# Optimization experiments

Hardware: AMD Instinct MI355X
Metric: run time of the kernel (lower is better)

## Reference

```python
import jax, jax.numpy as jnp
import numpy as np

B, T, D, DH, DFF = 4, 2048, 1024, 1024, 4096


def setup_inputs() -> dict:
    key = jax.random.key(0)
    ks = jax.random.split(key, 8)
    s = 0.02
    return {
        "x": jax.random.normal(ks[0], (B, T, D), jnp.float32),
        "ln1_g": jnp.ones((D,), jnp.float32),
        "ln1_b": jnp.zeros((D,), jnp.float32),
        "W_q": jax.random.normal(ks[1], (D, DH), jnp.float32) * s,
        "b_q": jnp.zeros((DH,), jnp.float32),
        "W_k": jax.random.normal(ks[2], (D, DH), jnp.float32) * s,
        "b_k": jnp.zeros((DH,), jnp.float32),
        "W_v": jax.random.normal(ks[3], (D, DH), jnp.float32) * s,
        "b_v": jnp.zeros((DH,), jnp.float32),
        "ln2_g": jnp.ones((D,), jnp.float32),
        "ln2_b": jnp.zeros((D,), jnp.float32),
        "W_in": jax.random.normal(ks[4], (D, DFF), jnp.float32) * s,
        "b_in": jnp.zeros((DFF,), jnp.float32),
        "W_out": jax.random.normal(ks[5], (DFF, D), jnp.float32) * s,
        "b_out": jnp.zeros((D,), jnp.float32),
    }


def _layernorm(x, g, b, eps=1e-5):
    mu = jnp.mean(x, axis=-1, keepdims=True)
    var = jnp.var(x, axis=-1, keepdims=True)
    return (x - mu) * jax.lax.rsqrt(var + eps) * g + b


def reference(x, ln1_g, ln1_b, W_q, b_q, W_k, b_k, W_v, b_v,
              ln2_g, ln2_b, W_in, b_in, W_out, b_out):
    # --- attention branch (pre-LN) ---
    h = _layernorm(x, ln1_g, ln1_b)                      # [B,T,D]
    Q = h @ W_q + b_q                                    # [B,T,DH]
    K = h @ W_k + b_k
    V = h @ W_v + b_v
    scale = 1.0 / jnp.sqrt(jnp.asarray(K.shape[-1], h.dtype))
    att = jnp.einsum("btd,bsd->bts", Q, K) * scale       # [B,T,T]
    # NOTE: source calls att.masked_fill(...) without assignment -> mask
    # is discarded; faithfully no causal mask applied here.
    att = jax.nn.softmax(att, axis=-1)
    attn_out = jnp.einsum("bts,bsd->btd", att, V)        # [B,T,DH]
    x = x + attn_out
    # --- MLP branch (pre-LN) ---
    h2 = _layernorm(x, ln2_g, ln2_b)
    ff = jax.nn.gelu(h2 @ W_in + b_in, approximate=False)
    x = x + (ff @ W_out + b_out)
    return x
```

## Files before the change

### kernel.cpp

```cpp
#include <hip/hip_runtime.h>
#include <hip/hip_bf16.h>

#define B_    4
#define T_    2048
#define D_    1024
#define DH_   1024
#define DFF_  4096
#define MTOT  (B_ * T_)

using f32x4  = __attribute__((ext_vector_type(4))) float;
using bf16x8 = __attribute__((ext_vector_type(8))) short;

__device__ __forceinline__ unsigned short f2bf(float f) {
    unsigned u = __builtin_bit_cast(unsigned, f);
    u += 0x7fffu + ((u >> 16) & 1u);
    return (unsigned short)(u >> 16);
}

__device__ __forceinline__ void gload16(const short* g, short* l) {
    __builtin_amdgcn_global_load_lds(
        (const __attribute__((address_space(1))) unsigned int*)g,
        (__attribute__((address_space(3))) unsigned int*)l, 16, 0, 0);
}

__global__ __launch_bounds__(256) void transp_f32_bf16(
    const float* __restrict__ src, short* __restrict__ dst, int K, int N) {
    __shared__ float tile[32][33];
    int tk = blockIdx.y * 32, tn = blockIdx.x * 32;
    int tx = threadIdx.x & 31, ty = threadIdx.x >> 5;
#pragma unroll
    for (int i = 0; i < 4; i++) {
        int r = ty + i * 8;
        tile[r][tx] = src[(size_t)(tk + r) * N + tn + tx];
    }
    __syncthreads();
#pragma unroll
    for (int i = 0; i < 4; i++) {
        int r = ty + i * 8;
        dst[(size_t)(tn + r) * K + tk + tx] = f2bf(tile[tx][r]);
    }
}

__global__ void copyv(const float* __restrict__ s, float* __restrict__ d, int n) {
    int i = blockIdx.x * blockDim.x + threadIdx.x;
    if (i < n) d[i] = s[i];
}

__global__ __launch_bounds__(256) void ln_rows(
    const float* __restrict__ x, const float* __restrict__ g,
    const float* __restrict__ bta, short* __restrict__ out) {
    int row = blockIdx.x;
    const float* xr = x + (size_t)row * D_;
    int t = threadIdx.x;
    float4 v = *(const float4*)(xr + t * 4);
    float s  = v.x + v.y + v.z + v.w;
    float s2 = v.x * v.x + v.y * v.y + v.z * v.z + v.w * v.w;
#pragma unroll
    for (int off = 1; off < 64; off <<= 1) {
        s  += __shfl_xor(s, off);
        s2 += __shfl_xor(s2, off);
    }
    __shared__ float as_[4], as2_[4];
    int wave = t >> 6, lane = t & 63;
    if (lane == 0) { as_[wave] = s; as2_[wave] = s2; }
    __syncthreads();
    s  = as_[0] + as_[1] + as_[2] + as_[3];
    s2 = as2_[0] + as2_[1] + as2_[2] + as2_[3];
    float mean = s * (1.0f / D_);
    float var  = s2 * (1.0f / D_) - mean * mean;
    float rstd = rsqrtf(var + 1e-5f);
    float4 gv = *(const float4*)(g + t * 4);
    float4 bv = *(const float4*)(bta + t * 4);
    short4 o;
    o.x = f2bf((v.x - mean) * rstd * gv.x + bv.x);
    o.y = f2bf((v.y - mean) * rstd * gv.y + bv.y);
    o.z = f2bf((v.z - mean) * rstd * gv.z + bv.z);
    o.w = f2bf((v.w - mean) * rstd * gv.w + bv.w);
    *(short4*)(out + (size_t)row * D_ + t * 4) = o;
}

__global__ __launch_bounds__(256) void softmax_rows(float* __restrict__ S) {
    size_t row = blockIdx.x;
    float* sr = S + row * (size_t)T_;
    int t = threadIdx.x;
    float4 v0 = *(const float4*)(sr + t * 4);
    float4 v1 = *(const float4*)(sr + 1024 + t * 4);
    const float c = 0.03125f;
    float vv[8] = {v0.x * c, v0.y * c, v0.z * c, v0.w * c,
                   v1.x * c, v1.y * c, v1.z * c, v1.w * c};
    float mx = -1e30f;
#pragma unroll
    for (int i = 0; i < 8; i++) mx = fmaxf(mx, vv[i]);
#pragma unroll
    for (int off = 1; off < 64; off <<= 1) mx = fmaxf(mx, __shfl_xor(mx, off));
    __shared__ float sm_[4], ss[4];
    int wave = t >> 6, lane = t & 63;
    if (lane == 0) sm_[wave] = mx;
    __syncthreads();
    mx = fmaxf(fmaxf(sm_[0], sm_[1]), fmaxf(sm_[2], sm_[3]));
    float sum = 0.f;
#pragma unroll
    for (int i = 0; i < 8; i++) { vv[i] = expf(vv[i] - mx); sum += vv[i]; }
#pragma unroll
    for (int off = 1; off < 64; off <<= 1) sum += __shfl_xor(sum, off);
    if (lane == 0) ss[wave] = sum;
    __syncthreads();
    sum = ss[0] + ss[1] + ss[2] + ss[3];
    float inv = 1.0f / sum;
    short* pr = (short*)sr;
    short4 oa, ob;
    oa.x = f2bf(vv[0] * inv); oa.y = f2bf(vv[1] * inv);
    oa.z = f2bf(vv[2] * inv); oa.w = f2bf(vv[3] * inv);
    ob.x = f2bf(vv[4] * inv); ob.y = f2bf(vv[5] * inv);
    ob.z = f2bf(vv[6] * inv); ob.w = f2bf(vv[7] * inv);
    *(short4*)(pr + t * 4) = oa;
    *(short4*)(pr + 1024 + t * 4) = ob;
}

#define TILE_SH 16384
template<int BIAS_MODE, int ACT, int RES, int OUT_BF16>
__global__ __launch_bounds__(512, 2) void gemm8(
    const short* __restrict__ A, int lda, long long sA,
    const short* __restrict__ Bt, int ldb, long long sB,
    void* __restrict__ C, int ldc, long long sC,
    const float* __restrict__ bias,
    const float* __restrict__ res, int ldr, long long sR,
    int K) {
    extern __shared__ short smem_[];
    short* shA = smem_;
    short* shB = smem_ + 2 * TILE_SH;

    int gx = gridDim.x, gy = gridDim.y;
    int n2d = gx * gy;
    int nwg = n2d * gridDim.z;
    int lid = blockIdx.x + gx * (blockIdx.y + gy * blockIdx.z);
    int q = nwg >> 3, rq = nwg & 7, xcd = lid & 7, i_ = lid >> 3;
    int nid = (xcd < rq ? xcd * (q + 1) : rq * (q + 1) + (xcd - rq) * q) + i_;
    int z = nid / n2d, r2d = nid % n2d;
    int sw = gy << 2;
    int strip = r2d / sw, rr = r2d % sw;
    int by = rr >> 2, bx = (strip << 2) + (rr & 3);

    int bm = by * 256, bn = bx * 256;
    const short* gA = A  + (size_t)z * sA + (size_t)bm * lda;
    const short* gB = Bt + (size_t)z * sB + (size_t)bn * ldb;
    int tid = threadIdx.x, lane = tid & 63, w = tid >> 6;
    int wr = w >> 2, wc = w & 3;

    int rbase = tid >> 3;
    int colb  = ((tid << 4) & 127) ^ ((rbase & 7) << 4);
    int col   = colb >> 1;
    const short* pA[4]; const short* pB[4];
#pragma unroll
    for (int c = 0; c < 4; c++) {
        pA[c] = gA + (size_t)(c * 64 + rbase) * lda + col;
        pB[c] = gB + (size_t)(c * 64 + rbase) * ldb + col;
    }
    int aoff[8], boff[4];
#pragma unroll
    for (int f = 0; f < 8; f++) {
        int row = wr * 128 + f * 16 + (lane & 15);
        aoff[f] = row * 128 + ((((lane >> 4) * 16)) ^ ((row & 7) << 4));
    }
#pragma unroll
    for (int f = 0; f < 4; f++) {
        int row = wc * 64 + f * 16 + (lane & 15);
        boff[f] = row * 128 + ((((lane >> 4) * 16)) ^ ((row & 7) << 4));
    }

    int nk = K >> 6;
    f32x4 acc[8][4] = {};

#pragma unroll
    for (int c = 0; c < 4; c++) {
        gload16(pA[c], shA + c * 4096 + tid * 8);
        gload16(pB[c], shB + c * 4096 + tid * 8);
    }
    asm volatile("s_waitcnt vmcnt(0)" ::: "memory");
    __builtin_amdgcn_s_barrier();

#define MF(r_, av) \
    acc[r_][0] = __builtin_amdgcn_mfma_f32_16x16x32_bf16(av, b0, acc[r_][0], 0, 0, 0); \
    acc[r_][1] = __builtin_amdgcn_mfma_f32_16x16x32_bf16(av, b1, acc[r_][1], 0, 0, 0); \
    acc[r_][2] = __builtin_amdgcn_mfma_f32_16x16x32_bf16(av, b2, acc[r_][2], 0, 0, 0); \
    acc[r_][3] = __builtin_amdgcn_mfma_f32_16x16x32_bf16(av, b3, acc[r_][3], 0, 0, 0);

    for (int t = 0; t < nk; t++) {
        const char* sA_ = (const char*)(shA + (t & 1) * TILE_SH);
        const char* sB_ = (const char*)(shB + (t & 1) * TILE_SH);
        short* wA = shA + ((t + 1) & 1) * TILE_SH;
        short* wB = shB + ((t + 1) & 1) * TILE_SH;
        int ks = (t + 1 < nk ? t + 1 : nk - 1) << 6;

        bf16x8 a0 = *(const bf16x8*)(sA_ + aoff[0]);
        bf16x8 a1 = *(const bf16x8*)(sA_ + aoff[1]);
        bf16x8 a2 = *(const bf16x8*)(sA_ + aoff[2]);
        bf16x8 a3 = *(const bf16x8*)(sA_ + aoff[3]);
        bf16x8 b0 = *(const bf16x8*)(sB_ + boff[0]);
        bf16x8 b1 = *(const bf16x8*)(sB_ + boff[1]);
        bf16x8 b2 = *(const bf16x8*)(sB_ + boff[2]);
        bf16x8 b3 = *(const bf16x8*)(sB_ + boff[3]);
        gload16(pA[0] + ks, wA + tid * 8);
        gload16(pA[2] + ks, wA + 2 * 4096 + tid * 8);
        __builtin_amdgcn_s_barrier();
        asm volatile("s_waitcnt lgkmcnt(0)" ::: "memory");
        __builtin_amdgcn_s_setprio(1);
        MF(0, a0) MF(1, a1) MF(2, a2) MF(3, a3)
        __builtin_amdgcn_s_setprio(0);
        asm volatile("s_waitcnt vmcnt(2)" ::: "memory");
        __builtin_amdgcn_s_barrier();

        a0 = *(const bf16x8*)(sA_ + aoff[4]);
        a1 = *(const bf16x8*)(sA_ + aoff[5]);
        a2 = *(const bf16x8*)(sA_ + aoff[6]);
        a3 = *(const bf16x8*)(sA_ + aoff[7]);
        gload16(pB[0] + ks, wB + tid * 8);
        gload16(pB[1] + ks, wB + 4096 + tid * 8);
        __builtin_amdgcn_s_barrier();
        asm volatile("s_waitcnt lgkmcnt(0)" ::: "memory");
        __builtin_amdgcn_s_setprio(1);
        MF(4, a0) MF(5, a1) MF(6, a2) MF(7, a3)
        __builtin_amdgcn_s_setprio(0);
        __builtin_amdgcn_s_barrier();

        a0 = *(const bf16x8*)(sA_ + (aoff[0] ^ 64));
        a1 = *(const bf16x8*)(sA_ + (aoff[1] ^ 64));
        a2 = *(const bf16x8*)(sA_ + (aoff[2] ^ 64));
        a3 = *(const bf16x8*)(sA_ + (aoff[3] ^ 64));
        b0 = *(const bf16x8*)(sB_ + (boff[0] ^ 64));
        b1 = *(const bf16x8*)(sB_ + (boff[1] ^ 64));
        b2 = *(const bf16x8*)(sB_ + (boff[2] ^ 64));
        b3 = *(const bf16x8*)(sB_ + (boff[3] ^ 64));
        gload16(pB[2] + ks, wB + 2 * 4096 + tid * 8);
        gload16(pB[3] + ks, wB + 3 * 4096 + tid * 8);
        __builtin_amdgcn_s_barrier();
        asm volatile("s_waitcnt lgkmcnt(0)" ::: "memory");
        __builtin_amdgcn_s_setprio(1);
        MF(0, a0) MF(1, a1) MF(2, a2) MF(3, a3)
        __builtin_amdgcn_s_setprio(0);
        __builtin_amdgcn_s_barrier();

        a0 = *(const bf16x8*)(sA_ + (aoff[4] ^ 64));
        a1 = *(const bf16x8*)(sA_ + (aoff[5] ^ 64));
        a2 = *(const bf16x8*)(sA_ + (aoff[6] ^ 64));
        a3 = *(const bf16x8*)(sA_ + (aoff[7] ^ 64));
        gload16(pA[1] + ks, wA + 4096 + tid * 8);
        gload16(pA[3] + ks, wA + 3 * 4096 + tid * 8);
        __builtin_amdgcn_s_barrier();
        asm volatile("s_waitcnt lgkmcnt(0)" ::: "memory");
        __builtin_amdgcn_s_setprio(1);
        MF(4, a0) MF(5, a1) MF(6, a2) MF(7, a3)
        __builtin_amdgcn_s_setprio(0);
        asm volatile("s_waitcnt vmcnt(2)" ::: "memory");
        __builtin_amdgcn_s_barrier();
    }
#undef MF
    asm volatile("s_waitcnt vmcnt(0)" ::: "memory");

    size_t zc = (size_t)z * (size_t)sC;
#pragma unroll
    for (int fr = 0; fr < 8; fr++) {
#pragma unroll
        for (int fn = 0; fn < 4; fn++) {
            int colc = bn + wc * 64 + fn * 16 + (lane & 15);
#pragma unroll
            for (int r_ = 0; r_ < 4; r_++) {
                int row = bm + wr * 128 + fr * 16 + (lane >> 4) * 4 + r_;
                float v = acc[fr][fn][r_];
                if (BIAS_MODE == 1) v += bias[colc];
                else if (BIAS_MODE == 2) v += bias[row];
                if (ACT == 1) v = 0.5f * v * (1.0f + erff(v * 0.70710678118654752f));
                if (RES) v += res[(size_t)z * sR + (size_t)row * ldr + colc];
                if (OUT_BF16) ((short*)C)[zc + (size_t)row * ldc + colc] = f2bf(v);
                else          ((float*)C)[zc + (size_t)row * ldc + colc] = v;
            }
        }
    }
}

#define SHBYTES (4 * TILE_SH * 2)

extern "C" void kernel_launch(void* const* d_in, const int* in_sizes, int n_in,
                              void* d_out, int out_size, void* d_ws, size_t ws_size,
                              hipStream_t stream) {
    const float* x    = (const float*)d_in[0];
    const float* ln1g = (const float*)d_in[1];
    const float* ln1b = (const float*)d_in[2];
    const float* Wq   = (const float*)d_in[3];
    const float* bq   = (const float*)d_in[4];
    const float* Wk   = (const float*)d_in[5];
    const float* bk   = (const float*)d_in[6];
    const float* Wv   = (const float*)d_in[7];
    const float* bv   = (const float*)d_in[8];
    const float* ln2g = (const float*)d_in[9];
    const float* ln2b = (const float*)d_in[10];
    const float* Win  = (const float*)d_in[11];
    const float* bin  = (const float*)d_in[12];
    const float* Wout = (const float*)d_in[13];
    const float* bout = (const float*)d_in[14];

    char* ws = (char*)d_ws;
    size_t off = 0;
    auto alloc = [&](size_t bytes) {
        void* p = ws + off;
        off += (bytes + 255) & ~(size_t)255;
        return p;
    };
    short* WqkT  = (short*)alloc((size_t)2048 * 1024 * 2);
    short* WvT   = (short*)alloc((size_t)1024 * 1024 * 2);
    short* WinT  = (short*)alloc((size_t)4096 * 1024 * 2);
    short* WoutT = (short*)alloc((size_t)1024 * 4096 * 2);
    float* bqk   = (float*)alloc((size_t)2048 * 4);
    short* h     = (short*)alloc((size_t)MTOT * 1024 * 2);
    short* QK    = (short*)alloc((size_t)MTOT * 2048 * 2);
    short* VT    = (short*)alloc((size_t)1024 * 8192 * 2);
    float* S     = (float*)alloc((size_t)4 * 2048 * 2048 * 4);
    float* x1    = (float*)alloc((size_t)MTOT * 1024 * 4);
    (void)ws_size; (void)in_sizes; (void)n_in; (void)out_size;

    hipFuncSetAttribute((const void*)gemm8<1,0,0,1>, hipFuncAttributeMaxDynamicSharedMemorySize, SHBYTES);
    hipFuncSetAttribute((const void*)gemm8<2,0,0,1>, hipFuncAttributeMaxDynamicSharedMemorySize, SHBYTES);
    hipFuncSetAttribute((const void*)gemm8<0,0,0,0>, hipFuncAttributeMaxDynamicSharedMemorySize, SHBYTES);
    hipFuncSetAttribute((const void*)gemm8<0,0,1,0>, hipFuncAttributeMaxDynamicSharedMemorySize, SHBYTES);
    hipFuncSetAttribute((const void*)gemm8<1,1,0,1>, hipFuncAttributeMaxDynamicSharedMemorySize, SHBYTES);
    hipFuncSetAttribute((const void*)gemm8<1,0,1,0>, hipFuncAttributeMaxDynamicSharedMemorySize, SHBYTES);

    transp_f32_bf16<<<dim3(32, 32), 256, 0, stream>>>(Wq, WqkT, 1024, 1024);
    transp_f32_bf16<<<dim3(32, 32), 256, 0, stream>>>(Wk, WqkT + (size_t)1024 * 1024, 1024, 1024);
    transp_f32_bf16<<<dim3(32, 32), 256, 0, stream>>>(Wv, WvT, 1024, 1024);
    transp_f32_bf16<<<dim3(128, 32), 256, 0, stream>>>(Win, WinT, 1024, 4096);
    transp_f32_bf16<<<dim3(32, 128), 256, 0, stream>>>(Wout, WoutT, 4096, 1024);
    copyv<<<4, 256, 0, stream>>>(bq, bqk, 1024);
    copyv<<<4, 256, 0, stream>>>(bk, bqk + 1024, 1024);

    ln_rows<<<MTOT, 256, 0, stream>>>(x, ln1g, ln1b, h);

    gemm8<1, 0, 0, 1><<<dim3(8, 32, 1), 512, SHBYTES, stream>>>(
        h, 1024, 0, WqkT, 1024, 0, QK, 2048, 0, bqk, nullptr, 0, 0, 1024);

    gemm8<2, 0, 0, 1><<<dim3(32, 4, 1), 512, SHBYTES, stream>>>(
        WvT, 1024, 0, h, 1024, 0, VT, 8192, 0, bv, nullptr, 0, 0, 1024);

    gemm8<0, 0, 0, 0><<<dim3(8, 8, 4), 512, SHBYTES, stream>>>(
        QK, 2048, 4194304LL, QK + 1024, 2048, 4194304LL,
        S, 2048, 4194304LL, nullptr, nullptr, 0, 0, 1024);

    softmax_rows<<<MTOT, 256, 0, stream>>>(S);

    gemm8<0, 0, 1, 0><<<dim3(4, 8, 4), 512, SHBYTES, stream>>>(
        (short*)S, 4096, 8388608LL, VT, 8192, 2048LL,
        x1, 1024, 2097152LL, nullptr, x, 1024, 2097152LL, 2048);

    ln_rows<<<MTOT, 256, 0, stream>>>(x1, ln2g, ln2b, h);

    short* ff = (short*)S;
    gemm8<1, 1, 0, 1><<<dim3(16, 32, 1), 512, SHBYTES, stream>>>(
        h, 1024, 0, WinT, 1024, 0, ff, 4096, 0, bin, nullptr, 0, 0, 1024);

    gemm8<1, 0, 1, 0><<<dim3(4, 32, 1), 512, SHBYTES, stream>>>(
        ff, 4096, 0, WoutT, 4096, 0, (float*)d_out, 1024, 0, bout,
        x1, 1024, 0, 4096);
}
```

Baseline: 432.7 us.

## Add narrow-N triple-buffered GEMM variant and write attention scores as bf16

```diff
diff --git a/kernel.cpp b/kernel.cpp
--- a/kernel.cpp
+++ b/kernel.cpp
@@ -15,6 +15,10 @@
     unsigned u = __builtin_bit_cast(unsigned, f);
     u += 0x7fffu + ((u >> 16) & 1u);
     return (unsigned short)(u >> 16);
+}
+__device__ __forceinline__ float bf2f(unsigned short h) {
+    unsigned u = ((unsigned)h) << 16;
+    return __builtin_bit_cast(float, u);
 }
 
 __device__ __forceinline__ void gload16(const short* g, short* l) {
@@ -79,15 +83,17 @@
     *(short4*)(out + (size_t)row * D_ + t * 4) = o;
 }
 
-__global__ __launch_bounds__(256) void softmax_rows(float* __restrict__ S) {
+__global__ __launch_bounds__(256) void softmax_rows_bf16(short* __restrict__ S) {
     size_t row = blockIdx.x;
-    float* sr = S + row * (size_t)T_;
+    short* sr = S + row * 4096;
     int t = threadIdx.x;
-    float4 v0 = *(const float4*)(sr + t * 4);
-    float4 v1 = *(const float4*)(sr + 1024 + t * 4);
+    short4 u0 = *(const short4*)(sr + t * 4);
+    short4 u1 = *(const short4*)(sr + 1024 + t * 4);
     const float c = 0.03125f;
-    float vv[8] = {v0.x * c, v0.y * c, v0.z * c, v0.w * c,
-                   v1.x * c, v1.y * c, v1.z * c, v1.w * c};
+    float vv[8] = {bf2f((unsigned short)u0.x) * c, bf2f((unsigned short)u0.y) * c,
+                   bf2f((unsigned short)u0.z) * c, bf2f((unsigned short)u0.w) * c,
+                   bf2f((unsigned short)u1.x) * c, bf2f((unsigned short)u1.y) * c,
+                   bf2f((unsigned short)u1.z) * c, bf2f((unsigned short)u1.w) * c};
     float mx = -1e30f;
 #pragma unroll
     for (int i = 0; i < 8; i++) mx = fmaxf(mx, vv[i]);
@@ -107,19 +113,17 @@
     __syncthreads();
     sum = ss[0] + ss[1] + ss[2] + ss[3];
     float inv = 1.0f / sum;
-    short* pr = (short*)sr;
     short4 oa, ob;
     oa.x = f2bf(vv[0] * inv); oa.y = f2bf(vv[1] * inv);
     oa.z = f2bf(vv[2] * inv); oa.w = f2bf(vv[3] * inv);
     ob.x = f2bf(vv[4] * inv); ob.y = f2bf(vv[5] * inv);
     ob.z = f2bf(vv[6] * inv); ob.w = f2bf(vv[7] * inv);
-    *(short4*)(pr + t * 4) = oa;
-    *(short4*)(pr + 1024 + t * 4) = ob;
-}
-
-#define TILE_SH 16384
-template<int BIAS_MODE, int ACT, int RES, int OUT_BF16>
-__global__ __launch_bounds__(512, 2) void gemm8(
+    *(short4*)(sr + t * 4) = oa;
+    *(short4*)(sr + 1024 + t * 4) = ob;
+}
+
+template<int NB, int BIAS_MODE, int ACT, int RES, int OUT_BF16>
+__global__ __launch_bounds__(512, 2) void gemmT(
     const short* __restrict__ A, int lda, long long sA,
     const short* __restrict__ Bt, int ldb, long long sB,
     void* __restrict__ C, int ldc, long long sC,
@@ -128,7 +132,8 @@
     int K) {
     extern __shared__ short smem_[];
     short* shA = smem_;
-    short* shB = smem_ + 2 * TILE_SH;
+    short* shB = smem_ + (NB == 4 ? 32768 : 49152);
+    const int SB = 4096 * NB;
 
     int gx = gridDim.x, gy = gridDim.y;
     int n2d = gx * gy;
@@ -141,21 +146,22 @@
     int strip = r2d / sw, rr = r2d % sw;
     int by = rr >> 2, bx = (strip << 2) + (rr & 3);
 
-    int bm = by * 256, bn = bx * 256;
+    int bm = by * 256, bn = bx * (64 * NB);
     const short* gA = A  + (size_t)z * sA + (size_t)bm * lda;
     const short* gB = Bt + (size_t)z * sB + (size_t)bn * ldb;
     int tid = threadIdx.x, lane = tid & 63, w = tid >> 6;
     int wr = w >> 2, wc = w & 3;
 
     int rbase = tid >> 3;
-    int colb  = ((tid << 4) & 127) ^ ((rbase & 7) << 4);
-    int col   = colb >> 1;
+    int gcol  = ((((tid & 7) << 4) ^ ((rbase & 7) << 4)) >> 1);
     const short* pA[4]; const short* pB[4];
 #pragma unroll
-    for (int c = 0; c < 4; c++) {
-        pA[c] = gA + (size_t)(c * 64 + rbase) * lda + col;
-        pB[c] = gB + (size_t)(c * 64 + rbase) * ldb + col;
-    }
+    for (int c = 0; c < 4; c++)
+        pA[c] = gA + (size_t)(c * 64 + rbase) * lda + gcol;
+#pragma unroll
+    for (int c = 0; c < NB; c++)
+        pB[c] = gB + (size_t)(c * 64 + rbase) * ldb + gcol;
+
     int aoff[8], boff[4];
 #pragma unroll
     for (int f = 0; f < 8; f++) {
@@ -163,106 +169,144 @@
         aoff[f] = row * 128 + ((((lane >> 4) * 16)) ^ ((row & 7) << 4));
     }
 #pragma unroll
-    for (int f = 0; f < 4; f++) {
-        int row = wc * 64 + f * 16 + (lane & 15);
+    for (int f = 0; f < NB; f++) {
+        int row = wc * (16 * NB) + f * 16 + (lane & 15);
         boff[f] = row * 128 + ((((lane >> 4) * 16)) ^ ((row & 7) << 4));
     }
 
     int nk = K >> 6;
-    f32x4 acc[8][4] = {};
-
-#pragma unroll
-    for (int c = 0; c < 4; c++) {
-        gload16(pA[c], shA + c * 4096 + tid * 8);
-        gload16(pB[c], shB + c * 4096 + tid * 8);
-    }
+    f32x4 acc[8][NB] = {};
+
+#define MFROW(r_, av) \
+    _Pragma("unroll") \
+    for (int n_ = 0; n_ < NB; n_++) \
+        acc[r_][n_] = __builtin_amdgcn_mfma_f32_16x16x32_bf16(av, bfv[n_], acc[r_][n_], 0, 0, 0);
+
+    if constexpr (NB == 4) {
+#pragma unroll
+        for (int c = 0; c < 4; c++) gload16(pA[c], shA + c * 4096 + tid * 8);
+#pragma unroll
+        for (int c = 0; c < 4; c++) gload16(pB[c], shB + c * 4096 + tid * 8);
+        asm volatile("s_waitcnt vmcnt(0)" ::: "memory");
+        __builtin_amdgcn_s_barrier();
+
+        for (int t = 0; t < nk; t++) {
+            const char* sA_ = (const char*)(shA + (t & 1) * 16384);
+            const char* sB_ = (const char*)(shB + (t & 1) * SB);
+            short* wA = shA + ((t + 1) & 1) * 16384;
+            short* wB = shB + ((t + 1) & 1) * SB;
+            int ks = (t + 1 < nk ? t + 1 : nk - 1) << 6;
+            bf16x8 af[4], bfv[4];
+
+#pragma unroll
+            for (int f = 0; f < 4; f++) af[f] = *(const bf16x8*)(sA_ + aoff[f]);
+#pragma unroll
+            for (int f = 0; f < 4; f++) bfv[f] = *(const bf16x8*)(sB_ + boff[f]);
+            gload16(pA[0] + ks, wA + tid * 8);
+            gload16(pA[2] + ks, wA + 2 * 4096 + tid * 8);
+            __builtin_amdgcn_s_barrier();
+            asm volatile("s_waitcnt lgkmcnt(0)" ::: "memory");
+            __builtin_amdgcn_s_setprio(1);
+            MFROW(0, af[0]) MFROW(1, af[1]) MFROW(2, af[2]) MFROW(3, af[3])
+            __builtin_amdgcn_s_setprio(0);
+            asm volatile("s_waitcnt vmcnt(2)" ::: "memory");
+            __builtin_amdgcn_s_barrier();
+#pragma unroll
+            for (int f = 0; f < 4; f++) af[f] = *(const bf16x8*)(sA_ + aoff[4 + f]);
+            gload16(pB[0] + ks, wB + tid * 8);
+            gload16(pB[1] + ks, wB + 4096 + tid * 8);
+            __builtin_amdgcn_s_barrier();
+            asm volatile("s_waitcnt lgkmcnt(0)" ::: "memory");
+            __builtin_amdgcn_s_setprio(1);
+            MFROW(4, af[0]) MFROW(5, af[1]) MFROW(6, af[2]) MFROW(7, af[3])
+            __builtin_amdgcn_s_setprio(0);
+            __builtin_amdgcn_s_barrier();
+#pragma unroll
+            for (int f = 0; f < 4; f++) af[f] = *(const bf16x8*)(sA_ + (aoff[f] ^ 64));
+#pragma unroll
+            for (int f = 0; f < 4; f++) bfv[f] = *(const bf16x8*)(sB_ + (boff[f] ^ 64));
+            gload16(pB[2] + ks, wB + 2 * 4096 + tid * 8);
+            gload16(pB[3] + ks, wB + 3 * 4096 + tid * 8);
+            __builtin_amdgcn_s_barrier();
+            asm volatile("s_waitcnt lgkmcnt(0)" ::: "memory");
+            __builtin_amdgcn_s_setprio(1);
+            MFROW(0, af[0]) MFROW(1, af[1]) MFROW(2, af[2]) MFROW(3, af[3])
+            __builtin_amdgcn_s_setprio(0);
+            __builtin_amdgcn_s_barrier();
+#pragma unroll
+            for (int f = 0; f < 4; f++) af[f] = *(const bf16x8*)(sA_ + (aoff[4 + f] ^ 64));
+            gload16(pA[1] + ks, wA + 4096 + tid * 8);
+            gload16(pA[3] + ks, wA + 3 * 4096 + tid * 8);
+            __builtin_amdgcn_s_barrier();
+            asm volatile("s_waitcnt lgkmcnt(0)" ::: "memory");
+            __builtin_amdgcn_s_setprio(1);
+            MFROW(4, af[0]) MFROW(5, af[1]) MFROW(6, af[2]) MFROW(7, af[3])
+            __builtin_amdgcn_s_setprio(0);
+            asm volatile("s_waitcnt vmcnt(2)" ::: "memory");
+            __builtin_amdgcn_s_barrier();
+        }
+    } else {
+#pragma unroll
+        for (int s = 0; s < 2; s++) {
+#pragma unroll
+            for (int c = 0; c < 4; c++)
+                gload16(pA[c] + s * 64, shA + s * 16384 + c * 4096 + tid * 8);
+#pragma unroll
+            for (int c = 0; c < 2; c++)
+                gload16(pB[c] + s * 64, shB + s * 8192 + c * 4096 + tid * 8);
+        }
+        asm volatile("s_waitcnt vmcnt(6)" ::: "memory");
+        __builtin_amdgcn_s_barrier();
+
+        for (int t = 0; t < nk; t++) {
+            int rs = t % 3, es = (t + 2) % 3;
+            const char* sA_ = (const char*)(shA + rs * 16384);
+            const char* sB_ = (const char*)(shB + rs * 8192);
+            short* wA = shA + es * 16384;
+            short* wB = shB + es * 8192;
+            int ks = (t + 2 < nk ? t + 2 : nk - 1) << 6;
+            bf16x8 af[8], bfv[2];
+
+#pragma unroll
+            for (int f = 0; f < 8; f++) af[f] = *(const bf16x8*)(sA_ + aoff[f]);
+#pragma unroll
+            for (int f = 0; f < 2; f++) bfv[f] = *(const bf16x8*)(sB_ + boff[f]);
+            gload16(pA[0] + ks, wA + tid * 8);
+            gload16(pA[1] + ks, wA + 4096 + tid * 8);
+            gload16(pA[2] + ks, wA + 2 * 4096 + tid * 8);
+            gload16(pA[3] + ks, wA + 3 * 4096 + tid * 8);
+            gload16(pB[0] + ks, wB + tid * 8);
+            gload16(pB[1] + ks, wB + 4096 + tid * 8);
+            __builtin_amdgcn_s_barrier();
+            asm volatile("s_waitcnt lgkmcnt(0)" ::: "memory");
+            __builtin_amdgcn_s_setprio(1);
+            MFROW(0, af[0]) MFROW(1, af[1]) MFROW(2, af[2]) MFROW(3, af[3])
+            MFROW(4, af[4]) MFROW(5, af[5]) MFROW(6, af[6]) MFROW(7, af[7])
+            __builtin_amdgcn_s_setprio(0);
+            __builtin_amdgcn_s_barrier();
+#pragma unroll
+            for (int f = 0; f < 8; f++) af[f] = *(const bf16x8*)(sA_ + (aoff[f] ^ 64));
+#pragma unroll
+            for (int f = 0; f < 2; f++) bfv[f] = *(const bf16x8*)(sB_ + (boff[f] ^ 64));
+            __builtin_amdgcn_s_barrier();
+            asm volatile("s_waitcnt lgkmcnt(0)" ::: "memory");
+            __builtin_amdgcn_s_setprio(1);
+            MFROW(0, af[0]) MFROW(1, af[1]) MFROW(2, af[2]) MFROW(3, af[3])
+            MFROW(4, af[4]) MFROW(5, af[5]) MFROW(6, af[6]) MFROW(7, af[7])
+            __builtin_amdgcn_s_setprio(0);
+            asm volatile("s_waitcnt vmcnt(6)" ::: "memory");
+            __builtin_amdgcn_s_barrier();
+        }
+    }
+#undef MFROW
     asm volatile("s_waitcnt vmcnt(0)" ::: "memory");
-    __builtin_amdgcn_s_barrier();
-
-#define MF(r_, av) \
-    acc[r_][0] = __builtin_amdgcn_mfma_f32_16x16x32_bf16(av, b0, acc[r_][0], 0, 0, 0); \
-    acc[r_][1] = __builtin_amdgcn_mfma_f32_16x16x32_bf16(av, b1, acc[r_][1], 0, 0, 0); \
-    acc[r_][2] = __builtin_amdgcn_mfma_f32_16x16x32_bf16(av, b2, acc[r_][2], 0, 0, 0); \
-    acc[r_][3] = __builtin_amdgcn_mfma_f32_16x16x32_bf16(av, b3, acc[r_][3], 0, 0, 0);
-
-    for (int t = 0; t < nk; t++) {
-        const char* sA_ = (const char*)(shA + (t & 1) * TILE_SH);
-        const char* sB_ = (const char*)(shB + (t & 1) * TILE_SH);
-        short* wA = shA + ((t + 1) & 1) * TILE_SH;
-        short* wB = shB + ((t + 1) & 1) * TILE_SH;
-        int ks = (t + 1 < nk ? t + 1 : nk - 1) << 6;
-
-        bf16x8 a0 = *(const bf16x8*)(sA_ + aoff[0]);
-        bf16x8 a1 = *(const bf16x8*)(sA_ + aoff[1]);
-        bf16x8 a2 = *(const bf16x8*)(sA_ + aoff[2]);
-        bf16x8 a3 = *(const bf16x8*)(sA_ + aoff[3]);
-        bf16x8 b0 = *(const bf16x8*)(sB_ + boff[0]);
-        bf16x8 b1 = *(const bf16x8*)(sB_ + boff[1]);
-        bf16x8 b2 = *(const bf16x8*)(sB_ + boff[2]);
-        bf16x8 b3 = *(const bf16x8*)(sB_ + boff[3]);
-        gload16(pA[0] + ks, wA + tid * 8);
-        gload16(pA[2] + ks, wA + 2 * 4096 + tid * 8);
-        __builtin_amdgcn_s_barrier();
-        asm volatile("s_waitcnt lgkmcnt(0)" ::: "memory");
-        __builtin_amdgcn_s_setprio(1);
-        MF(0, a0) MF(1, a1) MF(2, a2) MF(3, a3)
-        __builtin_amdgcn_s_setprio(0);
-        asm volatile("s_waitcnt vmcnt(2)" ::: "memory");
-        __builtin_amdgcn_s_barrier();
-
-        a0 = *(const bf16x8*)(sA_ + aoff[4]);
-        a1 = *(const bf16x8*)(sA_ + aoff[5]);
-        a2 = *(const bf16x8*)(sA_ + aoff[6]);
-        a3 = *(const bf16x8*)(sA_ + aoff[7]);
-        gload16(pB[0] + ks, wB + tid * 8);
-        gload16(pB[1] + ks, wB + 4096 + tid * 8);
-        __builtin_amdgcn_s_barrier();
-        asm volatile("s_waitcnt lgkmcnt(0)" ::: "memory");
-        __builtin_amdgcn_s_setprio(1);
-        MF(4, a0) MF(5, a1) MF(6, a2) MF(7, a3)
-        __builtin_amdgcn_s_setprio(0);
-        __builtin_amdgcn_s_barrier();
-
-        a0 = *(const bf16x8*)(sA_ + (aoff[0] ^ 64));
-        a1 = *(const bf16x8*)(sA_ + (aoff[1] ^ 64));
-        a2 = *(const bf16x8*)(sA_ + (aoff[2] ^ 64));
-        a3 = *(const bf16x8*)(sA_ + (aoff[3] ^ 64));
-        b0 = *(const bf16x8*)(sB_ + (boff[0] ^ 64));
-        b1 = *(const bf16x8*)(sB_ + (boff[1] ^ 64));
-        b2 = *(const bf16x8*)(sB_ + (boff[2] ^ 64));
-        b3 = *(const bf16x8*)(sB_ + (boff[3] ^ 64));
-        gload16(pB[2] + ks, wB + 2 * 4096 + tid * 8);
-        gload16(pB[3] + ks, wB + 3 * 4096 + tid * 8);
-        __builtin_amdgcn_s_barrier();
-        asm volatile("s_waitcnt lgkmcnt(0)" ::: "memory");
-        __builtin_amdgcn_s_setprio(1);
-        MF(0, a0) MF(1, a1) MF(2, a2) MF(3, a3)
-        __builtin_amdgcn_s_setprio(0);
-        __builtin_amdgcn_s_barrier();
-
-        a0 = *(const bf16x8*)(sA_ + (aoff[4] ^ 64));
-        a1 = *(const bf16x8*)(sA_ + (aoff[5] ^ 64));
-        a2 = *(const bf16x8*)(sA_ + (aoff[6] ^ 64));
-        a3 = *(const bf16x8*)(sA_ + (aoff[7] ^ 64));
-        gload16(pA[1] + ks, wA + 4096 + tid * 8);
-        gload16(pA[3] + ks, wA + 3 * 4096 + tid * 8);
-        __builtin_amdgcn_s_barrier();
-        asm volatile("s_waitcnt lgkmcnt(0)" ::: "memory");
-        __builtin_amdgcn_s_setprio(1);
-        MF(4, a0) MF(5, a1) MF(6, a2) MF(7, a3)
-        __builtin_amdgcn_s_setprio(0);
-        asm volatile("s_waitcnt vmcnt(2)" ::: "memory");
-        __builtin_amdgcn_s_barrier();
-    }
-#undef MF
-    asm volatile("s_waitcnt vmcnt(0)" ::: "memory");
 
     size_t zc = (size_t)z * (size_t)sC;
 #pragma unroll
     for (int fr = 0; fr < 8; fr++) {
 #pragma unroll
-        for (int fn = 0; fn < 4; fn++) {
-            int colc = bn + wc * 64 + fn * 16 + (lane & 15);
+        for (int fn = 0; fn < NB; fn++) {
+            int colc = bn + wc * (16 * NB) + fn * 16 + (lane & 15);
 #pragma unroll
             for (int r_ = 0; r_ < 4; r_++) {
                 int row = bm + wr * 128 + fr * 16 + (lane >> 4) * 4 + r_;
@@ -278,7 +322,8 @@
     }
 }
 
-#define SHBYTES (4 * TILE_SH * 2)
+#define SHB4 131072
+#define SHB2 147456
 
 extern "C" void kernel_launch(void* const* d_in, const int* in_sizes, int n_in,
                               void* d_out, int out_size, void* d_ws, size_t ws_size,
@@ -318,12 +363,12 @@
     float* x1    = (float*)alloc((size_t)MTOT * 1024 * 4);
     (void)ws_size; (void)in_sizes; (void)n_in; (void)out_size;
 
-    hipFuncSetAttribute((const void*)gemm8<1,0,0,1>, hipFuncAttributeMaxDynamicSharedMemorySize, SHBYTES);
-    hipFuncSetAttribute((const void*)gemm8<2,0,0,1>, hipFuncAttributeMaxDynamicSharedMemorySize, SHBYTES);
-    hipFuncSetAttribute((const void*)gemm8<0,0,0,0>, hipFuncAttributeMaxDynamicSharedMemorySize, SHBYTES);
-    hipFuncSetAttribute((const void*)gemm8<0,0,1,0>, hipFuncAttributeMaxDynamicSharedMemorySize, SHBYTES);
-    hipFuncSetAttribute((const void*)gemm8<1,1,0,1>, hipFuncAttributeMaxDynamicSharedMemorySize, SHBYTES);
-    hipFuncSetAttribute((const void*)gemm8<1,0,1,0>, hipFuncAttributeMaxDynamicSharedMemorySize, SHBYTES);
+    hipFuncSetAttribute((const void*)gemmT<4,1,0,0,1>, hipFuncAttributeMaxDynamicSharedMemorySize, SHB4);
+    hipFuncSetAttribute((const void*)gemmT<4,0,0,0,1>, hipFuncAttributeMaxDynamicSharedMemorySize, SHB4);
+    hipFuncSetAttribute((const void*)gemmT<4,1,1,0,1>, hipFuncAttributeMaxDynamicSharedMemorySize, SHB4);
+    hipFuncSetAttribute((const void*)gemmT<2,2,0,0,1>, hipFuncAttributeMaxDynamicSharedMemorySize, SHB2);
+    hipFuncSetAttribute((const void*)gemmT<2,0,0,1,0>, hipFuncAttributeMaxDynamicSharedMemorySize, SHB2);
+    hipFuncSetAttribute((const void*)gemmT<2,1,0,1,0>, hipFuncAttributeMaxDynamicSharedMemorySize, SHB2);
 
     transp_f32_bf16<<<dim3(32, 32), 256, 0, stream>>>(Wq, WqkT, 1024, 1024);
     transp_f32_bf16<<<dim3(32, 32), 256, 0, stream>>>(Wk, WqkT + (size_t)1024 * 1024, 1024, 1024);
@@ -335,29 +380,29 @@
 
     ln_rows<<<MTOT, 256, 0, stream>>>(x, ln1g, ln1b, h);
 
-    gemm8<1, 0, 0, 1><<<dim3(8, 32, 1), 512, SHBYTES, stream>>>(
+    gemmT<4, 1, 0, 0, 1><<<dim3(8, 32, 1), 512, SHB4, stream>>>(
         h, 1024, 0, WqkT, 1024, 0, QK, 2048, 0, bqk, nullptr, 0, 0, 1024);
 
-    gemm8<2, 0, 0, 1><<<dim3(32, 4, 1), 512, SHBYTES, stream>>>(
+    gemmT<2, 2, 0, 0, 1><<<dim3(64, 4, 1), 512, SHB2, stream>>>(
         WvT, 1024, 0, h, 1024, 0, VT, 8192, 0, bv, nullptr, 0, 0, 1024);
 
-    gemm8<0, 0, 0, 0><<<dim3(8, 8, 4), 512, SHBYTES, stream>>>(
+    gemmT<4, 0, 0, 0, 1><<<dim3(8, 8, 4), 512, SHB4, stream>>>(
         QK, 2048, 4194304LL, QK + 1024, 2048, 4194304LL,
-        S, 2048, 4194304LL, nullptr, nullptr, 0, 0, 1024);
-
-    softmax_rows<<<MTOT, 256, 0, stream>>>(S);
-
-    gemm8<0, 0, 1, 0><<<dim3(4, 8, 4), 512, SHBYTES, stream>>>(
+        (short*)S, 4096, 8388608LL, nullptr, nullptr, 0, 0, 1024);
+
+    softmax_rows_bf16<<<MTOT, 256, 0, stream>>>((short*)S);
+
+    gemmT<2, 0, 0, 1, 0><<<dim3(8, 8, 4), 512, SHB2, stream>>>(
         (short*)S, 4096, 8388608LL, VT, 8192, 2048LL,
         x1, 1024, 2097152LL, nullptr, x, 1024, 2097152LL, 2048);
 
     ln_rows<<<MTOT, 256, 0, stream>>>(x1, ln2g, ln2b, h);
 
     short* ff = (short*)S;
-    gemm8<1, 1, 0, 1><<<dim3(16, 32, 1), 512, SHBYTES, stream>>>(
+    gemmT<4, 1, 1, 0, 1><<<dim3(16, 32, 1), 512, SHB4, stream>>>(
         h, 1024, 0, WinT, 1024, 0, ff, 4096, 0, bin, nullptr, 0, 0, 1024);
 
-    gemm8<1, 0, 1, 0><<<dim3(4, 32, 1), 512, SHBYTES, stream>>>(
+    gemmT<2, 1, 0, 1, 0><<<dim3(8, 32, 1), 512, SHB2, stream>>>(
         ff, 4096, 0, WoutT, 4096, 0, (float*)d_out, 1024, 0, bout,
         x1, 1024, 0, 4096);
 }
```

After: 399.8 us. 7.6% less time.
